# Performance work log

Hardware: AMD Instinct MI355X
Metric: run time of the kernel (lower is better)

## Reference

```python
import jax, jax.numpy as jnp
import numpy as np

HEAD = 8
KERNEL = 7


def setup_inputs() -> dict:
    key = jax.random.key(0)
    ks = jax.random.split(key, 5)
    N, C, H, W = 2, 256, 56, 56
    scale = 1.0 / np.sqrt(C)
    queries = jax.random.normal(ks[0], (N, C, H, W), jnp.float32)
    key_t = jax.random.normal(ks[1], (N, C, H, W), jnp.float32)
    in_proj_w = jax.random.normal(ks[2], (3 * C, C), jnp.float32) * scale
    in_proj_b = jnp.zeros((3 * C,), jnp.float32)
    out_proj_w = jax.random.normal(ks[3], (C, C), jnp.float32) * scale
    out_proj_b = jnp.zeros((C,), jnp.float32)
    pos_enc = jnp.full((1, 1), float(KERNEL ** 2), jnp.float32)  # nn.Parameter([[kernel**2]])
    return dict(queries=queries, key=key_t, pos_enc=pos_enc,
                in_proj_w=in_proj_w, in_proj_b=in_proj_b,
                out_proj_w=out_proj_w, out_proj_b=out_proj_b)


def reference(queries, key, pos_enc, in_proj_w, in_proj_b, out_proj_w, out_proj_b):
    N, C, H, W = queries.shape
    k2 = KERNEL * KERNEL
    c = (KERNEL - 1) // 2
    # zero-pad key and extract k x k neighborhoods (same ordering as unfold: row-major i*k+j)
    kp = jnp.pad(key, ((0, 0), (0, 0), (c, c), (c, c)))
    patches = jnp.stack([kp[:, :, i:i + H, j:j + W]
                         for i in range(KERNEL) for j in range(KERNEL)], axis=-1)  # (N,C,H,W,k2)
    kv = patches.reshape(N, C, H * W, k2) + pos_enc[0, 0]   # scalar position bias
    kv = kv.transpose(0, 2, 3, 1)                            # (N, P, k2, C), P = H*W pixels
    q = queries.reshape(N, C, H * W).transpose(0, 2, 1)      # (N, P, C)

    Wq, Wk, Wv = jnp.split(in_proj_w, 3, axis=0)
    bq, bk, bv = jnp.split(in_proj_b, 3)
    d = C // HEAD
    qh = (q @ Wq.T + bq).reshape(N, H * W, HEAD, d)
    kh = (kv @ Wk.T + bk).reshape(N, H * W, k2, HEAD, d)
    vh = (kv @ Wv.T + bv).reshape(N, H * W, k2, HEAD, d)

    scores = jnp.einsum('nphd,npkhd->nphk', qh, kh) / jnp.sqrt(jnp.asarray(d, qh.dtype))
    attn = jax.nn.softmax(scores, axis=-1)
    o = jnp.einsum('nphk,npkhd->nphd', attn, vh).reshape(N, H * W, C)
    out = o @ out_proj_w.T + out_proj_b                       # (N, P, C)
    return out.transpose(0, 2, 1).reshape(N, C, H, W)
```

## Files before the change

kernel.cpp:

```cpp
#include <hip/hip_runtime.h>
#include <stdint.h>

#define HW 56
#define P 3136
#define C 256
#define CP (C*P)

typedef float  f32x4  __attribute__((ext_vector_type(4)));
typedef short  short8 __attribute__((ext_vector_type(8)));

__device__ __forceinline__ unsigned short f2bf(float f) {
    uint32_t u = __float_as_uint(f);
    uint32_t r = (u + 0x7fffu + ((u >> 16) & 1u)) >> 16;
    return (unsigned short)r;
}
__device__ __forceinline__ float bl(uint32_t u) { return __uint_as_float(u << 16); }
__device__ __forceinline__ float bh(uint32_t u) { return __uint_as_float(u & 0xffff0000u); }

__device__ __forceinline__ void gload16(const void* g, const void* l) {
    __builtin_amdgcn_global_load_lds(
        (const __attribute__((address_space(1))) uint32_t*)g,
        (__attribute__((address_space(3))) uint32_t*)l, 16, 0, 0);
}

__global__ __launch_bounds__(256) void wconv_kernel(const float* __restrict__ ipw,
                                                    const float* __restrict__ opw,
                                                    unsigned short* __restrict__ Wb) {
    int i4 = blockIdx.x * 256 + threadIdx.x;
    const float4* src = (i4 < 49152) ? (const float4*)ipw : (const float4*)opw;
    int idx = (i4 < 49152) ? i4 : i4 - 49152;
    float4 v = src[idx];
    ((ushort4*)Wb)[i4] = make_ushort4(f2bf(v.x), f2bf(v.y), f2bf(v.z), f2bf(v.w));
}

__global__ __launch_bounds__(256) void tconv_kernel(const float* __restrict__ queries,
                                                    const float* __restrict__ key,
                                                    unsigned short* __restrict__ Qt,
                                                    unsigned short* __restrict__ Kt) {
    __shared__ float Ls[64][65];
    int t = threadIdx.x;
    int p0 = blockIdx.x * 64, ci0 = blockIdx.y * 64;
    int n = blockIdx.z & 1, which = blockIdx.z >> 1;
    const float* X = (which ? key : queries) + (size_t)n * CP;
    unsigned short* Xt = (which ? Kt : Qt) + (size_t)n * P * 256;

    int c = t & 63, r0 = t >> 6;
    #pragma unroll
    for (int rr = 0; rr < 16; ++rr) {
        int cil = r0 * 16 + rr;
        Ls[c][cil] = X[(size_t)(ci0 + cil) * P + p0 + c];
    }
    __syncthreads();
    int pl = t >> 2, cch = (t & 3) * 16;
    uint32_t us[8];
    #pragma unroll
    for (int j = 0; j < 8; ++j) {
        float lo = Ls[pl][cch + 2 * j], hi = Ls[pl][cch + 2 * j + 1];
        us[j] = (uint32_t)f2bf(lo) | ((uint32_t)f2bf(hi) << 16);
    }
    uint4* dst = (uint4*)(Xt + (size_t)(p0 + pl) * 256 + ci0 + cch);
    dst[0] = make_uint4(us[0], us[1], us[2], us[3]);
    dst[1] = make_uint4(us[4], us[5], us[6], us[7]);
}

__global__ __launch_bounds__(256) void vb_kernel(const float* __restrict__ ipw,
                                                 const float* __restrict__ ipb,
                                                 const float* __restrict__ pos,
                                                 float* __restrict__ vbc) {
    int w = threadIdx.x >> 6, lane = threadIdx.x & 63;
    float pe = pos[0];
    #pragma unroll
    for (int i = 0; i < 4; ++i) {
        int r = blockIdx.x * 16 + w * 4 + i;
        const float* row = ipw + (size_t)(512 + r) * 256;
        float s = row[lane] + row[lane + 64] + row[lane + 128] + row[lane + 192];
        #pragma unroll
        for (int off = 32; off; off >>= 1) s += __shfl_xor(s, off);
        if (lane == 0) vbc[r] = fmaf(pe, s, ipb[512 + r]);
    }
}

__global__ __launch_bounds__(256) void ob_kernel(const float* __restrict__ opw,
                                                 const float* __restrict__ opb,
                                                 const float* __restrict__ vbc,
                                                 float* __restrict__ obc) {
    int w = threadIdx.x >> 6, lane = threadIdx.x & 63;
    #pragma unroll
    for (int i = 0; i < 4; ++i) {
        int co = blockIdx.x * 16 + w * 4 + i;
        const float* row = opw + (size_t)co * 256;
        float s = row[lane] * vbc[lane] + row[lane + 64] * vbc[lane + 64]
                + row[lane + 128] * vbc[lane + 128] + row[lane + 192] * vbc[lane + 192];
        #pragma unroll
        for (int off = 32; off; off >>= 1) s += __shfl_xor(s, off);
        if (lane == 0) obc[co] = s + opb[co];
    }
}

__device__ __forceinline__ void gemm_core(const unsigned short* __restrict__ A,
                                          const unsigned short* __restrict__ B,
                                          int p0, unsigned short* As, unsigned short* Bs,
                                          f32x4 acc[4][2]) {
    int tid = threadIdx.x;
    int wid = __builtin_amdgcn_readfirstlane(tid >> 6);
    int lane = tid & 63;
    int wr = wid >> 1, wc = wid & 1;

    #pragma unroll
    for (int m = 0; m < 4; ++m)
        #pragma unroll
        for (int j = 0; j < 2; ++j) acc[m][j] = (f32x4){0.f, 0.f, 0.f, 0.f};

    for (int k0 = 0; k0 < 256; k0 += 32) {
        #pragma unroll
        for (int i = 0; i < 2; ++i) {
            int ch = i * 256 + (wid << 6) + lane;
            int row = ch >> 2;
            int g = (ch & 3) ^ ((row >> 1) & 3);
            gload16(A + (size_t)row * 256 + k0 + g * 8, (const char*)As + i * 4096 + wid * 1024);
        }
        {
            int ch = (wid << 6) + lane;
            int row = ch >> 2;
            int g = (ch & 3) ^ ((row >> 1) & 3);
            gload16(B + (size_t)(p0 + row) * 256 + k0 + g * 8, (const char*)Bs + wid * 1024);
        }
        __syncthreads();
        short8 af[4], bfr[2];
        #pragma unroll
        for (int m = 0; m < 4; ++m) {
            int col = (wr << 6) + m * 16 + (lane & 15);
            int phys = (lane >> 4) ^ ((col >> 1) & 3);
            af[m] = *(const short8*)((const char*)As + col * 64 + phys * 16);
        }
        #pragma unroll
        for (int j = 0; j < 2; ++j) {
            int pl = (wc << 5) + j * 16 + (lane & 15);
            int phys = (lane >> 4) ^ ((pl >> 1) & 3);
            bfr[j] = *(const short8*)((const char*)Bs + pl * 64 + phys * 16);
        }
        #pragma unroll
        for (int m = 0; m < 4; ++m)
            #pragma unroll
            for (int j = 0; j < 2; ++j)
                acc[m][j] = __builtin_amdgcn_mfma_f32_16x16x32_bf16(af[m], bfr[j], acc[m][j], 0, 0, 0);
        __syncthreads();
    }
}

__global__ __launch_bounds__(256) void proj_mfma(const unsigned short* __restrict__ Wb,
                                                 const unsigned short* __restrict__ Qt,
                                                 const unsigned short* __restrict__ Kt,
                                                 const float* __restrict__ ipb,
                                                 unsigned short* __restrict__ Qb,
                                                 unsigned short* __restrict__ Kb,
                                                 unsigned short* __restrict__ Vb) {
    __shared__ __align__(16) unsigned short As[4096];
    __shared__ __align__(16) unsigned short Bs[2048];
    int ty = blockIdx.y, n = blockIdx.z;
    int p0 = blockIdx.x * 64;
    int proj = ty >> 1;
    int co0 = ty * 128;
    const unsigned short* A = Wb + (size_t)co0 * 256;
    const unsigned short* B = (proj == 0 ? Qt : Kt) + (size_t)n * P * 256;
    unsigned short* outb = (proj == 0 ? Qb : (proj == 1 ? Kb : Vb)) + (size_t)n * 8 * P * 32;
    int col0 = (ty & 1) * 128;

    f32x4 acc[4][2];
    gemm_core(A, B, p0, As, Bs, acc);

    int lane = threadIdx.x & 63;
    int wid = threadIdx.x >> 6;
    int wr = wid >> 1, wc = wid & 1;
    #pragma unroll
    for (int m = 0; m < 4; ++m)
        #pragma unroll
        for (int j = 0; j < 2; ++j) {
            int col = col0 + (wr << 6) + m * 16 + (lane >> 4) * 4;
            int p   = p0 + (wc << 5) + j * 16 + (lane & 15);
            float v0 = acc[m][j][0], v1 = acc[m][j][1], v2 = acc[m][j][2], v3 = acc[m][j][3];
            if (proj == 0) {
                int cg = co0 + (wr << 6) + m * 16 + (lane >> 4) * 4;
                v0 += ipb[cg]; v1 += ipb[cg + 1]; v2 += ipb[cg + 2]; v3 += ipb[cg + 3];
            }
            int h = col >> 5, d = col & 31;
            ushort4 u = make_ushort4(f2bf(v0), f2bf(v1), f2bf(v2), f2bf(v3));
            *(ushort4*)(outb + ((size_t)(h * P + p)) * 32 + d) = u;
        }
}

__global__ __launch_bounds__(64) void attn_kernel(const unsigned short* __restrict__ Qb,
                                                  const unsigned short* __restrict__ Kb,
                                                  const unsigned short* __restrict__ Vb,
                                                  unsigned short* __restrict__ Ot) {
    int lane = threadIdx.x;
    int p = blockIdx.x * 64 + lane;
    int h = blockIdx.y, n = blockIdx.z;
    const float scale = 0.17677669529663687f;

    const uint4* qr = (const uint4*)(Qb + ((size_t)((n * 8 + h) * P + p)) * 32);
    float q[32];
    #pragma unroll
    for (int c = 0; c < 4; ++c) {
        uint4 u = qr[c];
        q[c*8+0] = bl(u.x); q[c*8+1] = bh(u.x); q[c*8+2] = bl(u.y); q[c*8+3] = bh(u.y);
        q[c*8+4] = bl(u.z); q[c*8+5] = bh(u.z); q[c*8+6] = bl(u.w); q[c*8+7] = bh(u.w);
    }
    const unsigned short* Kbase = Kb + (size_t)(n * 8 + h) * P * 32;
    const unsigned short* Vbase = Vb + (size_t)(n * 8 + h) * P * 32;
    int y = p / HW, x = p % HW;

    float o[32];
    #pragma unroll
    for (int d = 0; d < 32; ++d) o[d] = 0.f;
    float l = 0.f;

    #pragma unroll
    for (int dy = -3; dy <= 3; ++dy) {
        #pragma unroll
        for (int dx = -3; dx <= 3; ++dx) {
            int yy = y + dy, xx = x + dx;
            bool in = (yy >= 0) & (yy < HW) & (xx >= 0) & (xx < HW);
            int pnb = in ? (p + dy * HW + dx) : p;
            const uint4* kr = (const uint4*)(Kbase + (size_t)pnb * 32);
            float dot = 0.f;
            #pragma unroll
            for (int c = 0; c < 4; ++c) {
                uint4 u = kr[c];
                dot = fmaf(q[c*8+0], bl(u.x), dot); dot = fmaf(q[c*8+1], bh(u.x), dot);
                dot = fmaf(q[c*8+2], bl(u.y), dot); dot = fmaf(q[c*8+3], bh(u.y), dot);
                dot = fmaf(q[c*8+4], bl(u.z), dot); dot = fmaf(q[c*8+5], bh(u.z), dot);
                dot = fmaf(q[c*8+6], bh(u.w), dot); dot = fmaf(q[c*8+6], bl(u.w), dot);
            }
            dot = 0.f;
            #pragma unroll
            for (int c = 0; c < 4; ++c) {
                uint4 u = kr[c];
                dot = fmaf(q[c*8+0], bl(u.x), dot); dot = fmaf(q[c*8+1], bh(u.x), dot);
                dot = fmaf(q[c*8+2], bl(u.y), dot); dot = fmaf(q[c*8+3], bh(u.y), dot);
                dot = fmaf(q[c*8+4], bl(u.z), dot); dot = fmaf(q[c*8+5], bh(u.z), dot);
                dot = fmaf(q[c*8+6], bl(u.w), dot); dot = fmaf(q[c*8+7], bh(u.w), dot);
            }
            float e = __expf(dot * scale);
            l += in ? e : 1.0f;
            float w = in ? e : 0.0f;
            const uint4* vr = (const uint4*)(Vbase + (size_t)pnb * 32);
            #pragma unroll
            for (int c = 0; c < 4; ++c) {
                uint4 u = vr[c];
                o[c*8+0] = fmaf(w, bl(u.x), o[c*8+0]); o[c*8+1] = fmaf(w, bh(u.x), o[c*8+1]);
                o[c*8+2] = fmaf(w, bl(u.y), o[c*8+2]); o[c*8+3] = fmaf(w, bh(u.y), o[c*8+3]);
                o[c*8+4] = fmaf(w, bl(u.z), o[c*8+4]); o[c*8+5] = fmaf(w, bh(u.z), o[c*8+5]);
                o[c*8+6] = fmaf(w, bl(u.w), o[c*8+6]); o[c*8+7] = fmaf(w, bh(u.w), o[c*8+7]);
            }
        }
    }
    float inv = __builtin_amdgcn_rcpf(l);
    uint32_t us[16];
    #pragma unroll
    for (int j = 0; j < 16; ++j)
        us[j] = (uint32_t)f2bf(o[2*j] * inv) | ((uint32_t)f2bf(o[2*j+1] * inv) << 16);
    uint4* dst = (uint4*)(Ot + (size_t)(n * P + p) * 256 + h * 32);
    #pragma unroll
    for (int c = 0; c < 4; ++c) dst[c] = make_uint4(us[4*c], us[4*c+1], us[4*c+2], us[4*c+3]);
}

__global__ __launch_bounds__(256) void outproj_mfma(const unsigned short* __restrict__ Wb,
                                                    const unsigned short* __restrict__ Ot,
                                                    const float* __restrict__ obc,
                                                    float* __restrict__ out) {
    __shared__ __align__(16) unsigned short As[4096];
    __shared__ __align__(16) unsigned short Bs[2048];
    int n = blockIdx.z;
    int p0 = blockIdx.x * 64;
    int co0 = blockIdx.y * 128;
    const unsigned short* A = Wb + (size_t)(768 + co0) * 256;
    const unsigned short* B = Ot + (size_t)n * P * 256;

    f32x4 acc[4][2];
    gemm_core(A, B, p0, As, Bs, acc);

    int lane = threadIdx.x & 63;
    int wid = threadIdx.x >> 6;
    int wr = wid >> 1, wc = wid & 1;
    #pragma unroll
    for (int m = 0; m < 4; ++m)
        #pragma unroll
        for (int j = 0; j < 2; ++j) {
            int co = co0 + (wr << 6) + m * 16 + (lane >> 4) * 4;
            int p  = p0 + (wc << 5) + j * 16 + (lane & 15);
            #pragma unroll
            for (int i = 0; i < 4; ++i)
                out[(size_t)n * CP + (size_t)(co + i) * P + p] = acc[m][j][i] + obc[co + i];
        }
}

extern "C" void kernel_launch(void* const* d_in, const int* in_sizes, int n_in,
                              void* d_out, int out_size, void* d_ws, size_t ws_size,
                              hipStream_t stream) {
    (void)in_sizes; (void)n_in; (void)out_size; (void)ws_size;
    const float* queries = (const float*)d_in[0];
    const float* key     = (const float*)d_in[1];
    const float* pos     = (const float*)d_in[2];
    const float* ipw     = (const float*)d_in[3];
    const float* ipb     = (const float*)d_in[4];
    const float* opw     = (const float*)d_in[5];
    const float* opb     = (const float*)d_in[6];
    float* out = (float*)d_out;

    unsigned short* us = (unsigned short*)d_ws;
    const size_t SZ = (size_t)2 * P * 256;
    unsigned short* Qt = us;
    unsigned short* Kt = us + SZ;
    unsigned short* Qb = us + 2 * SZ;
    unsigned short* Kb = us + 3 * SZ;
    unsigned short* Vb = us + 4 * SZ;
    unsigned short* Ot = us + 5 * SZ;
    unsigned short* Wb = us + 6 * SZ;
    float* fc  = (float*)(us + 6 * SZ + 262144);
    float* vbc = fc;
    float* obc = fc + 256;

    hipLaunchKernelGGL(wconv_kernel, dim3(256), dim3(256), 0, stream, ipw, opw, Wb);
    hipLaunchKernelGGL(tconv_kernel, dim3(49, 4, 4), dim3(256), 0, stream, queries, key, Qt, Kt);
    hipLaunchKernelGGL(vb_kernel, dim3(16), dim3(256), 0, stream, ipw, ipb, pos, vbc);
    hipLaunchKernelGGL(ob_kernel, dim3(16), dim3(256), 0, stream, opw, opb, vbc, obc);
    hipLaunchKernelGGL(proj_mfma, dim3(49, 6, 2), dim3(256), 0, stream,
                       Wb, Qt, Kt, ipb, Qb, Kb, Vb);
    hipLaunchKernelGGL(attn_kernel, dim3(49, 8, 2), dim3(64), 0, stream, Qb, Kb, Vb, Ot);
    hipLaunchKernelGGL(outproj_mfma, dim3(49, 2, 2), dim3(256), 0, stream, Wb, Ot, obc, out);
}
```

Baseline: 126.8 us.

## Split attention taps across four waves and fuse small bias kernels

The attention kernel now runs 256 threads per block. Each of four waves computes exp-scores for a quarter of the 49 taps into shared memory, then each wave accumulates 8 of the 32 head dimensions over all taps. This aims to raise parallelism and occupancy over the old one-wave-per-64-pixels design. The old code also computed the dot product twice, and that redundant pass is removed. The vb bias computation is folded into the weight-conversion kernel and the ob bias is computed inside outproj, which drops two launches; in exchange, each outproj block recomputes its 128 bias values.

```diff
diff --git a/kernel.cpp b/kernel.cpp
--- a/kernel.cpp
+++ b/kernel.cpp
@@ -23,14 +23,33 @@
         (__attribute__((address_space(3))) uint32_t*)l, 16, 0, 0);
 }
 
-__global__ __launch_bounds__(256) void wconv_kernel(const float* __restrict__ ipw,
-                                                    const float* __restrict__ opw,
-                                                    unsigned short* __restrict__ Wb) {
-    int i4 = blockIdx.x * 256 + threadIdx.x;
-    const float4* src = (i4 < 49152) ? (const float4*)ipw : (const float4*)opw;
-    int idx = (i4 < 49152) ? i4 : i4 - 49152;
-    float4 v = src[idx];
-    ((ushort4*)Wb)[i4] = make_ushort4(f2bf(v.x), f2bf(v.y), f2bf(v.z), f2bf(v.w));
+__global__ __launch_bounds__(256) void wconv_vb_kernel(const float* __restrict__ ipw,
+                                                       const float* __restrict__ opw,
+                                                       const float* __restrict__ ipb,
+                                                       const float* __restrict__ pos,
+                                                       unsigned short* __restrict__ Wb,
+                                                       float* __restrict__ vbc) {
+    int bx = blockIdx.x;
+    if (bx < 256) {
+        int i4 = bx * 256 + threadIdx.x;
+        const float4* src = (i4 < 49152) ? (const float4*)ipw : (const float4*)opw;
+        int idx = (i4 < 49152) ? i4 : i4 - 49152;
+        float4 v = src[idx];
+        ((ushort4*)Wb)[i4] = make_ushort4(f2bf(v.x), f2bf(v.y), f2bf(v.z), f2bf(v.w));
+    } else {
+        int b = bx - 256;
+        int w = threadIdx.x >> 6, lane = threadIdx.x & 63;
+        float pe = pos[0];
+        #pragma unroll
+        for (int i = 0; i < 4; ++i) {
+            int r = b * 16 + w * 4 + i;
+            const float* row = ipw + (size_t)(512 + r) * 256;
+            float s = row[lane] + row[lane + 64] + row[lane + 128] + row[lane + 192];
+            #pragma unroll
+            for (int off = 32; off; off >>= 1) s += __shfl_xor(s, off);
+            if (lane == 0) vbc[r] = fmaf(pe, s, ipb[512 + r]);
+        }
+    }
 }
 
 __global__ __launch_bounds__(256) void tconv_kernel(const float* __restrict__ queries,
@@ -61,40 +80,6 @@
     uint4* dst = (uint4*)(Xt + (size_t)(p0 + pl) * 256 + ci0 + cch);
     dst[0] = make_uint4(us[0], us[1], us[2], us[3]);
     dst[1] = make_uint4(us[4], us[5], us[6], us[7]);
-}
-
-__global__ __launch_bounds__(256) void vb_kernel(const float* __restrict__ ipw,
-                                                 const float* __restrict__ ipb,
-                                                 const float* __restrict__ pos,
-                                                 float* __restrict__ vbc) {
-    int w = threadIdx.x >> 6, lane = threadIdx.x & 63;
-    float pe = pos[0];
-    #pragma unroll
-    for (int i = 0; i < 4; ++i) {
-        int r = blockIdx.x * 16 + w * 4 + i;
-        const float* row = ipw + (size_t)(512 + r) * 256;
-        float s = row[lane] + row[lane + 64] + row[lane + 128] + row[lane + 192];
-        #pragma unroll
-        for (int off = 32; off; off >>= 1) s += __shfl_xor(s, off);
-        if (lane == 0) vbc[r] = fmaf(pe, s, ipb[512 + r]);
-    }
-}
-
-__global__ __launch_bounds__(256) void ob_kernel(const float* __restrict__ opw,
-                                                 const float* __restrict__ opb,
-                                                 const float* __restrict__ vbc,
-                                                 float* __restrict__ obc) {
-    int w = threadIdx.x >> 6, lane = threadIdx.x & 63;
-    #pragma unroll
-    for (int i = 0; i < 4; ++i) {
-        int co = blockIdx.x * 16 + w * 4 + i;
-        const float* row = opw + (size_t)co * 256;
-        float s = row[lane] * vbc[lane] + row[lane + 64] * vbc[lane + 64]
-                + row[lane + 128] * vbc[lane + 128] + row[lane + 192] * vbc[lane + 192];
-        #pragma unroll
-        for (int off = 32; off; off >>= 1) s += __shfl_xor(s, off);
-        if (lane == 0) obc[co] = s + opb[co];
-    }
 }
 
 __device__ __forceinline__ void gemm_core(const unsigned short* __restrict__ A,
@@ -189,14 +174,49 @@
         }
 }
 
-__global__ __launch_bounds__(64) void attn_kernel(const unsigned short* __restrict__ Qb,
-                                                  const unsigned short* __restrict__ Kb,
-                                                  const unsigned short* __restrict__ Vb,
-                                                  unsigned short* __restrict__ Ot) {
-    int lane = threadIdx.x;
+__constant__ const float kScale = 0.17677669529663687f;
+
+template<int T0, int T1>
+__device__ __forceinline__ void tap_range(const float* __restrict__ q,
+                                          const unsigned short* __restrict__ Kbase,
+                                          int p, int y, int x,
+                                          float* __restrict__ ws_col, float& l) {
+    #pragma unroll
+    for (int t = T0; t < T1; ++t) {
+        int dy = t / 7 - 3, dx = t % 7 - 3;
+        int yy = y + dy, xx = x + dx;
+        bool in = (yy >= 0) & (yy < HW) & (xx >= 0) & (xx < HW);
+        int pnb = in ? (p + dy * HW + dx) : p;
+        const uint4* kr = (const uint4*)(Kbase + (size_t)pnb * 32);
+        float dot = 0.f;
+        #pragma unroll
+        for (int c = 0; c < 4; ++c) {
+            uint4 u = kr[c];
+            dot = fmaf(q[c*8+0], bl(u.x), dot); dot = fmaf(q[c*8+1], bh(u.x), dot);
+            dot = fmaf(q[c*8+2], bl(u.y), dot); dot = fmaf(q[c*8+3], bh(u.y), dot);
+            dot = fmaf(q[c*8+4], bl(u.z), dot); dot = fmaf(q[c*8+5], bh(u.z), dot);
+            dot = fmaf(q[c*8+6], bl(u.w), dot); dot = fmaf(q[c*8+7], bh(u.w), dot);
+        }
+        float e = in ? __expf(dot * kScale) : 0.f;
+        l += in ? e : 1.0f;
+        ws_col[t * 64] = e;
+    }
+}
+
+__global__ __launch_bounds__(256) void attn_kernel(const unsigned short* __restrict__ Qb,
+                                                   const unsigned short* __restrict__ Kb,
+                                                   const unsigned short* __restrict__ Vb,
+                                                   unsigned short* __restrict__ Ot) {
+    __shared__ float Ws[49][64];
+    __shared__ float Lp[4][64];
+    int tid = threadIdx.x;
+    int lane = tid & 63, wave = tid >> 6;
     int p = blockIdx.x * 64 + lane;
     int h = blockIdx.y, n = blockIdx.z;
-    const float scale = 0.17677669529663687f;
+    int y = p / HW, x = p % HW;
+
+    const unsigned short* Kbase = Kb + (size_t)(n * 8 + h) * P * 32;
+    const unsigned short* Vbase = Vb + (size_t)(n * 8 + h) * P * 32;
 
     const uint4* qr = (const uint4*)(Qb + ((size_t)((n * 8 + h) * P + p)) * 32);
     float q[32];
@@ -206,92 +226,84 @@
         q[c*8+0] = bl(u.x); q[c*8+1] = bh(u.x); q[c*8+2] = bl(u.y); q[c*8+3] = bh(u.y);
         q[c*8+4] = bl(u.z); q[c*8+5] = bh(u.z); q[c*8+6] = bl(u.w); q[c*8+7] = bh(u.w);
     }
-    const unsigned short* Kbase = Kb + (size_t)(n * 8 + h) * P * 32;
-    const unsigned short* Vbase = Vb + (size_t)(n * 8 + h) * P * 32;
-    int y = p / HW, x = p % HW;
-
-    float o[32];
-    #pragma unroll
-    for (int d = 0; d < 32; ++d) o[d] = 0.f;
+
     float l = 0.f;
-
-    #pragma unroll
-    for (int dy = -3; dy <= 3; ++dy) {
-        #pragma unroll
-        for (int dx = -3; dx <= 3; ++dx) {
-            int yy = y + dy, xx = x + dx;
-            bool in = (yy >= 0) & (yy < HW) & (xx >= 0) & (xx < HW);
-            int pnb = in ? (p + dy * HW + dx) : p;
-            const uint4* kr = (const uint4*)(Kbase + (size_t)pnb * 32);
-            float dot = 0.f;
-            #pragma unroll
-            for (int c = 0; c < 4; ++c) {
-                uint4 u = kr[c];
-                dot = fmaf(q[c*8+0], bl(u.x), dot); dot = fmaf(q[c*8+1], bh(u.x), dot);
-                dot = fmaf(q[c*8+2], bl(u.y), dot); dot = fmaf(q[c*8+3], bh(u.y), dot);
-                dot = fmaf(q[c*8+4], bl(u.z), dot); dot = fmaf(q[c*8+5], bh(u.z), dot);
-                dot = fmaf(q[c*8+6], bh(u.w), dot); dot = fmaf(q[c*8+6], bl(u.w), dot);
-            }
-            dot = 0.f;
-            #pragma unroll
-            for (int c = 0; c < 4; ++c) {
-                uint4 u = kr[c];
-                dot = fmaf(q[c*8+0], bl(u.x), dot); dot = fmaf(q[c*8+1], bh(u.x), dot);
-                dot = fmaf(q[c*8+2], bl(u.y), dot); dot = fmaf(q[c*8+3], bh(u.y), dot);
-                dot = fmaf(q[c*8+4], bl(u.z), dot); dot = fmaf(q[c*8+5], bh(u.z), dot);
-                dot = fmaf(q[c*8+6], bl(u.w), dot); dot = fmaf(q[c*8+7], bh(u.w), dot);
-            }
-            float e = __expf(dot * scale);
-            l += in ? e : 1.0f;
-            float w = in ? e : 0.0f;
-            const uint4* vr = (const uint4*)(Vbase + (size_t)pnb * 32);
-            #pragma unroll
-            for (int c = 0; c < 4; ++c) {
-                uint4 u = vr[c];
-                o[c*8+0] = fmaf(w, bl(u.x), o[c*8+0]); o[c*8+1] = fmaf(w, bh(u.x), o[c*8+1]);
-                o[c*8+2] = fmaf(w, bl(u.y), o[c*8+2]); o[c*8+3] = fmaf(w, bh(u.y), o[c*8+3]);
-                o[c*8+4] = fmaf(w, bl(u.z), o[c*8+4]); o[c*8+5] = fmaf(w, bh(u.z), o[c*8+5]);
-                o[c*8+6] = fmaf(w, bl(u.w), o[c*8+6]); o[c*8+7] = fmaf(w, bh(u.w), o[c*8+7]);
-            }
-        }
-    }
-    float inv = __builtin_amdgcn_rcpf(l);
-    uint32_t us[16];
-    #pragma unroll
-    for (int j = 0; j < 16; ++j)
+    float* ws_col = &Ws[0][lane];
+    if      (wave == 0) tap_range< 0, 13>(q, Kbase, p, y, x, ws_col, l);
+    else if (wave == 1) tap_range<13, 25>(q, Kbase, p, y, x, ws_col, l);
+    else if (wave == 2) tap_range<25, 37>(q, Kbase, p, y, x, ws_col, l);
+    else                tap_range<37, 49>(q, Kbase, p, y, x, ws_col, l);
+    Lp[wave][lane] = l;
+    __syncthreads();
+
+    float lt = Lp[0][lane] + Lp[1][lane] + Lp[2][lane] + Lp[3][lane];
+    float inv = __builtin_amdgcn_rcpf(lt);
+
+    int d0 = wave * 8;
+    float o[8] = {0.f, 0.f, 0.f, 0.f, 0.f, 0.f, 0.f, 0.f};
+    #pragma unroll
+    for (int t = 0; t < 49; ++t) {
+        int dy = t / 7 - 3, dx = t % 7 - 3;
+        int yy = y + dy, xx = x + dx;
+        bool in = (yy >= 0) & (yy < HW) & (xx >= 0) & (xx < HW);
+        int pnb = in ? (p + dy * HW + dx) : p;
+        float w = Ws[t][lane];
+        uint4 u = *(const uint4*)(Vbase + (size_t)pnb * 32 + d0);
+        o[0] = fmaf(w, bl(u.x), o[0]); o[1] = fmaf(w, bh(u.x), o[1]);
+        o[2] = fmaf(w, bl(u.y), o[2]); o[3] = fmaf(w, bh(u.y), o[3]);
+        o[4] = fmaf(w, bl(u.z), o[4]); o[5] = fmaf(w, bh(u.z), o[5]);
+        o[6] = fmaf(w, bl(u.w), o[6]); o[7] = fmaf(w, bh(u.w), o[7]);
+    }
+    uint32_t us[4];
+    #pragma unroll
+    for (int j = 0; j < 4; ++j)
         us[j] = (uint32_t)f2bf(o[2*j] * inv) | ((uint32_t)f2bf(o[2*j+1] * inv) << 16);
-    uint4* dst = (uint4*)(Ot + (size_t)(n * P + p) * 256 + h * 32);
-    #pragma unroll
-    for (int c = 0; c < 4; ++c) dst[c] = make_uint4(us[4*c], us[4*c+1], us[4*c+2], us[4*c+3]);
+    *(uint4*)(Ot + (size_t)(n * P + p) * 256 + h * 32 + d0) =
+        make_uint4(us[0], us[1], us[2], us[3]);
 }
 
 __global__ __launch_bounds__(256) void outproj_mfma(const unsigned short* __restrict__ Wb,
                                                     const unsigned short* __restrict__ Ot,
-                                                    const float* __restrict__ obc,
+                                                    const float* __restrict__ opw,
+                                                    const float* __restrict__ opb,
+                                                    const float* __restrict__ vbc,
                                                     float* __restrict__ out) {
     __shared__ __align__(16) unsigned short As[4096];
     __shared__ __align__(16) unsigned short Bs[2048];
+    __shared__ float obc_s[128];
+    int tid = threadIdx.x;
     int n = blockIdx.z;
     int p0 = blockIdx.x * 64;
     int co0 = blockIdx.y * 128;
+
+    {
+        int r = tid >> 1, half = tid & 1;
+        const float* row = opw + (size_t)(co0 + r) * 256 + half * 128;
+        const float* vh = vbc + half * 128;
+        float s = 0.f;
+        #pragma unroll 8
+        for (int i = 0; i < 128; ++i) s = fmaf(row[i], vh[i], s);
+        s += __shfl_xor(s, 1);
+        if (half == 0) obc_s[r] = s + opb[co0 + r];
+    }
+
     const unsigned short* A = Wb + (size_t)(768 + co0) * 256;
     const unsigned short* B = Ot + (size_t)n * P * 256;
-
     f32x4 acc[4][2];
     gemm_core(A, B, p0, As, Bs, acc);
 
-    int lane = threadIdx.x & 63;
-    int wid = threadIdx.x >> 6;
+    int lane = tid & 63;
+    int wid = tid >> 6;
     int wr = wid >> 1, wc = wid & 1;
     #pragma unroll
     for (int m = 0; m < 4; ++m)
         #pragma unroll
         for (int j = 0; j < 2; ++j) {
-            int co = co0 + (wr << 6) + m * 16 + (lane >> 4) * 4;
+            int col = (wr << 6) + m * 16 + (lane >> 4) * 4;
             int p  = p0 + (wc << 5) + j * 16 + (lane & 15);
             #pragma unroll
             for (int i = 0; i < 4; ++i)
-                out[(size_t)n * CP + (size_t)(co + i) * P + p] = acc[m][j][i] + obc[co + i];
+                out[(size_t)n * CP + (size_t)(co0 + col + i) * P + p] = acc[m][j][i] + obc_s[col + i];
         }
 }
 
@@ -317,16 +329,15 @@
     unsigned short* Vb = us + 4 * SZ;
     unsigned short* Ot = us + 5 * SZ;
     unsigned short* Wb = us + 6 * SZ;
-    float* fc  = (float*)(us + 6 * SZ + 262144);
-    float* vbc = fc;
-    float* obc = fc + 256;
-
-    hipLaunchKernelGGL(wconv_kernel, dim3(256), dim3(256), 0, stream, ipw, opw, Wb);
-    hipLaunchKernelGGL(tconv_kernel, dim3(49, 4, 4), dim3(256), 0, stream, queries, key, Qt, Kt);
-    hipLaunchKernelGGL(vb_kernel, dim3(16), dim3(256), 0, stream, ipw, ipb, pos, vbc);
-    hipLaunchKernelGGL(ob_kernel, dim3(16), dim3(256), 0, stream, opw, opb, vbc, obc);
+    float* vbc = (float*)(us + 6 * SZ + 262144);
+
+    hipLaunchKernelGGL(wconv_vb_kernel, dim3(272), dim3(256), 0, stream,
+                       ipw, opw, ipb, pos, Wb, vbc);
+    hipLaunchKernelGGL(tconv_kernel, dim3(49, 4, 4), dim3(256), 0, stream,
+                       queries, key, Qt, Kt);
     hipLaunchKernelGGL(proj_mfma, dim3(49, 6, 2), dim3(256), 0, stream,
                        Wb, Qt, Kt, ipb, Qb, Kb, Vb);
-    hipLaunchKernelGGL(attn_kernel, dim3(49, 8, 2), dim3(64), 0, stream, Qb, Kb, Vb, Ot);
-    hipLaunchKernelGGL(outproj_mfma, dim3(49, 2, 2), dim3(256), 0, stream, Wb, Ot, obc, out);
-}
+    hipLaunchKernelGGL(attn_kernel, dim3(49, 8, 2), dim3(256), 0, stream, Qb, Kb, Vb, Ot);
+    hipLaunchKernelGGL(outproj_mfma, dim3(49, 2, 2), dim3(256), 0, stream,
+                       Wb, Ot, opw, opb, vbc, out);
+}
```

Result: no change. 126.5 us (-0.2%).
